# Kernel optimization log

Hardware: AMD Instinct MI355X
Metric: run time of the kernel (lower is better)

## Reference

```python
import jax, jax.numpy as jnp
import numpy as np

B, N, C = 4, 4096, 2048
EPS = 1e-5  # torch.nn.LayerNorm default


def setup_inputs() -> dict:
    key = jax.random.key(0)
    kx, = jax.random.split(key, 1)
    x = jax.random.normal(kx, (B, N, C), dtype=jnp.float32)
    gamma = jnp.ones((C,), dtype=jnp.float32)   # LayerNorm weight
    beta = jnp.zeros((C,), dtype=jnp.float32)   # LayerNorm bias
    return {"x": x, "gamma": gamma, "beta": beta}


def reference(x, gamma, beta):
    # The original repeats x to (B,N,N,C), applies a (no-op on the diagonal)
    # triu mask, FFTs every row over C, and extracts the (n,n) diagonal.
    # The diagonal rows are exactly the unmasked originals, so this equals:
    #   LayerNorm(real(fft(x, axis=-1)))
    y = jnp.fft.fft(x, axis=-1).real  # (B,N,C)
    mu = jnp.mean(y, axis=-1, keepdims=True)
    var = jnp.mean(jnp.square(y - mu), axis=-1, keepdims=True)  # biased, as torch LN
    return (y - mu) * jax.lax.rsqrt(var + EPS) * gamma + beta
```

## Files before the change

kernel.cpp:

```cpp
#include <hip/hip_runtime.h>
#include <math.h>


#define TPB 256
#define CD  2048

__device__ __forceinline__ float2 cadd(float2 a, float2 b){ return make_float2(a.x+b.x, a.y+b.y); }
__device__ __forceinline__ float2 csub(float2 a, float2 b){ return make_float2(a.x-b.x, a.y-b.y); }

__device__ __forceinline__ void dft8(const float2* z, float2* y)
{
    const float C8 = 0.70710678118654752440f;
    float2 a0=cadd(z[0],z[4]), a1=cadd(z[1],z[5]), a2=cadd(z[2],z[6]), a3=cadd(z[3],z[7]);
    float2 b0=csub(z[0],z[4]), b1=csub(z[1],z[5]), b2=csub(z[2],z[6]), b3=csub(z[3],z[7]);
    float2 t1=make_float2(C8*(b1.x+b1.y), C8*(b1.y-b1.x));
    float2 t2=make_float2(b2.y, -b2.x);
    float2 t3=make_float2(C8*(b3.y-b3.x), -C8*(b3.x+b3.y));
    {
        float pr=a0.x+a2.x, pi=a0.y+a2.y, mr=a0.x-a2.x, mi=a0.y-a2.y;
        float qr=a1.x+a3.x, qi=a1.y+a3.y, nr=a1.x-a3.x, ni=a1.y-a3.y;
        y[0]=make_float2(pr+qr,pi+qi); y[2]=make_float2(mr+ni,mi-nr);
        y[4]=make_float2(pr-qr,pi-qi); y[6]=make_float2(mr-ni,mi+nr);
    }
    {
        float pr=b0.x+t2.x, pi=b0.y+t2.y, mr=b0.x-t2.x, mi=b0.y-t2.y;
        float qr=t1.x+t3.x, qi=t1.y+t3.y, nr=t1.x-t3.x, ni=t1.y-t3.y;
        y[1]=make_float2(pr+qr,pi+qi); y[3]=make_float2(mr+ni,mi-nr);
        y[5]=make_float2(pr-qr,pi-qi); y[7]=make_float2(mr-ni,mi+nr);
    }
}

template<int S_, int OFFM>
__device__ __forceinline__ void r8_store(float2* Lw, const float2* y, int p)
{
    Lw[0] = y[0];
    if (S_ == 64 && p == 0) {
#pragma unroll
        for (int r = 1; r < 8; ++r) Lw[OFFM*r] = y[r];
        return;
    }
    const float th = -6.28318530717958647692f * ((float)S_ / 2048.0f);
    float s1, c1;
    __sincosf(th * (float)p, &s1, &c1);
    float cr=c1, sr=s1;
    Lw[OFFM] = make_float2(c1*y[1].x - s1*y[1].y, c1*y[1].y + s1*y[1].x);
#pragma unroll
    for (int r = 2; r < 8; ++r) {
        float cn = cr*c1 - sr*s1, sn = sr*c1 + cr*s1;
        cr=cn; sr=sn;
        Lw[OFFM*r] = make_float2(cr*y[r].x - sr*y[r].y, cr*y[r].y + sr*y[r].x);
    }
}

__global__ __launch_bounds__(TPB, 8) void fourier_ln_kernel(
    const float* __restrict__ x,
    const float* __restrict__ gamma,
    const float* __restrict__ beta,
    float* __restrict__ out)
{
    __shared__ float2 L[2304];
    __shared__ float rmem[20];

    const int t  = threadIdx.x;
    const int t8 = t >> 3;
    const long long row0 = 2LL * (long long)blockIdx.x;
    const float* __restrict__ x0 = x + row0 * CD;
    const float* __restrict__ x1 = x0 + CD;

    float2 z[8], y[8];
#pragma unroll
    for (int r = 0; r < 8; ++r) {
        const int k = t + 256*r;
        z[r] = make_float2(x0[k], x1[k]);
    }

    float2* const Lr = L + (t + t8);

    dft8(z, y);
    r8_store<1, 1>(L + 9*t, y, t);
    __syncthreads();
#pragma unroll
    for (int r = 0; r < 8; ++r) z[r] = Lr[288*r];
    __syncthreads();

    dft8(z, y);
    r8_store<8, 9>(L + ((t & 7) + 72*t8), y, t8);
    __syncthreads();
#pragma unroll
    for (int r = 0; r < 8; ++r) z[r] = Lr[288*r];
    __syncthreads();

    dft8(z, y);
    {
        const int q = t & 63, p = t >> 6;
        r8_store<64, 72>(L + (q + (q >> 3) + 576*p), y, p);
    }
    __syncthreads();
#pragma unroll
    for (int r = 0; r < 8; ++r) z[r] = Lr[288*r];
    __syncthreads();

    float2 Z[8];
    {
        float pr=z[0].x+z[4].x, pi=z[0].y+z[4].y, mr=z[0].x-z[4].x, mi=z[0].y-z[4].y;
        float qr=z[2].x+z[6].x, qi=z[2].y+z[6].y, nr=z[2].x-z[6].x, ni=z[2].y-z[6].y;
        Z[0]=make_float2(pr+qr,pi+qi); Z[2]=make_float2(mr+ni,mi-nr);
        Z[4]=make_float2(pr-qr,pi-qi); Z[6]=make_float2(mr-ni,mi+nr);
    }
    {
        float pr=z[1].x+z[5].x, pi=z[1].y+z[5].y, mr=z[1].x-z[5].x, mi=z[1].y-z[5].y;
        float qr=z[3].x+z[7].x, qi=z[3].y+z[7].y, nr=z[3].x-z[7].x, ni=z[3].y-z[7].y;
        Z[1]=make_float2(pr+qr,pi+qi); Z[3]=make_float2(mr+ni,mi-nr);
        Z[5]=make_float2(pr-qr,pi-qi); Z[7]=make_float2(mr-ni,mi+nr);
    }
#pragma unroll
    for (int j = 0; j < 8; ++j) Lr[288*j] = Z[j];
    __syncthreads();

    float y0v[8], y1v[8];
    float s0=0.f, ss0=0.f, s1=0.f, ss1=0.f;
    const float2* const Ls = L + (4*t + (t >> 1));
#pragma unroll
    for (int h = 0; h < 2; ++h) {
#pragma unroll
        for (int c = 0; c < 4; ++c) {
            const int k  = 4*t + 1024*h + c;
            const int rv = (CD - k) & (CD - 1);
            float2 zk = Ls[c + 1152*h];
            float2 zr = L[rv + (rv >> 3)];
            float a = 0.5f*(zk.x + zr.x);
            float b = 0.5f*(zk.y + zr.y);
            const int i = 4*h + c;
            y0v[i]=a; y1v[i]=b;
            s0+=a; ss0+=a*a; s1+=b; ss1+=b*b;
        }
    }

#pragma unroll
    for (int off = 32; off > 0; off >>= 1) {
        s0  += __shfl_down(s0,  off, 64);
        ss0 += __shfl_down(ss0, off, 64);
        s1  += __shfl_down(s1,  off, 64);
        ss1 += __shfl_down(ss1, off, 64);
    }
    const int wave = t >> 6;
    if ((t & 63) == 0) {
        rmem[4*wave+0]=s0; rmem[4*wave+1]=ss0; rmem[4*wave+2]=s1; rmem[4*wave+3]=ss1;
    }
    __syncthreads();
    if (t == 0) {
        float S0=0.f, SS0=0.f, S1=0.f, SS1=0.f;
#pragma unroll
        for (int w = 0; w < 4; ++w) {
            S0+=rmem[4*w+0]; SS0+=rmem[4*w+1]; S1+=rmem[4*w+2]; SS1+=rmem[4*w+3];
        }
        const float inv = 1.0f/(float)CD;
        float m0=S0*inv, m1=S1*inv;
        rmem[16]=m0; rmem[17]=rsqrtf(SS0*inv - m0*m0 + 1e-5f);
        rmem[18]=m1; rmem[19]=rsqrtf(SS1*inv - m1*m1 + 1e-5f);
    }
    __syncthreads();
    const float mu0=rmem[16], r0=rmem[17], mu1=rmem[18], r1=rmem[19];

    const float4* gv = (const float4*)gamma;
    const float4* bv = (const float4*)beta;
    float4* o0 = (float4*)(out + row0*CD);
    float4* o1 = (float4*)(out + (row0+1)*CD);
#pragma unroll
    for (int h = 0; h < 2; ++h) {
        const int i4 = t + 256*h;
        float4 g  = gv[i4];
        float4 be = bv[i4];
        float4 v0, v1;
        v0.x=(y0v[4*h+0]-mu0)*r0*g.x+be.x; v0.y=(y0v[4*h+1]-mu0)*r0*g.y+be.y;
        v0.z=(y0v[4*h+2]-mu0)*r0*g.z+be.z; v0.w=(y0v[4*h+3]-mu0)*r0*g.w+be.w;
        v1.x=(y1v[4*h+0]-mu1)*r1*g.x+be.x; v1.y=(y1v[4*h+1]-mu1)*r1*g.y+be.y;
        v1.z=(y1v[4*h+2]-mu1)*r1*g.z+be.z; v1.w=(y1v[4*h+3]-mu1)*r1*g.w+be.w;
        o0[i4]=v0; o1[i4]=v1;
    }
}

extern "C" void kernel_launch(void* const* d_in, const int* in_sizes, int n_in,
                              void* d_out, int out_size, void* d_ws, size_t ws_size,
                              hipStream_t stream) {
    (void)in_sizes; (void)n_in; (void)d_ws; (void)ws_size; (void)out_size;
    const float* x     = (const float*)d_in[0];
    const float* gamma = (const float*)d_in[1];
    const float* beta  = (const float*)d_in[2];
    float* out = (float*)d_out;

    const int total_rows = 4 * 4096;
    const int blocks = total_rows / 2;
    fourier_ln_kernel<<<blocks, TPB, 0, stream>>>(x, gamma, beta, out);
}
```

Before: 232.7 us.

## Pair conjugate FFT bins across lanes to drop final LDS round trip and barriers

The last radix-4 stage now reads from a permuted column index so that adjacent lanes hold bins k and N-k. The real-part split uses a lane shuffle instead of writing the spectrum back to LDS and re-reading it, which removes two barriers and an LDS pass. The final statistics are reduced redundantly by every thread, dropping another barrier, and twiddles are computed by squaring instead of a serial recurrence. In exchange, global stores become scalar and strided rather than float4, and gamma/beta are loaded per element.

```diff
diff --git a/kernel.cpp b/kernel.cpp
--- a/kernel.cpp
+++ b/kernel.cpp
@@ -42,14 +42,18 @@
     const float th = -6.28318530717958647692f * ((float)S_ / 2048.0f);
     float s1, c1;
     __sincosf(th * (float)p, &s1, &c1);
-    float cr=c1, sr=s1;
-    Lw[OFFM] = make_float2(c1*y[1].x - s1*y[1].y, c1*y[1].y + s1*y[1].x);
+    const float c2 = c1*c1 - s1*s1, s2 = 2.0f*c1*s1;
+    const float c4 = c2*c2 - s2*s2, s4 = 2.0f*c2*s2;
+    const float c3 = c1*c2 - s1*s2, s3 = s1*c2 + c1*s2;
+    const float c5 = c1*c4 - s1*s4, s5 = s1*c4 + c1*s4;
+    const float c6 = c2*c4 - s2*s4, s6 = s2*c4 + c2*s4;
+    const float c7 = c3*c4 - s3*s4, s7 = s3*c4 + c3*s4;
+    const float cw[8] = {1.f, c1, c2, c3, c4, c5, c6, c7};
+    const float sw[8] = {0.f, s1, s2, s3, s4, s5, s6, s7};
 #pragma unroll
-    for (int r = 2; r < 8; ++r) {
-        float cn = cr*c1 - sr*s1, sn = sr*c1 + cr*s1;
-        cr=cn; sr=sn;
-        Lw[OFFM*r] = make_float2(cr*y[r].x - sr*y[r].y, cr*y[r].y + sr*y[r].x);
-    }
+    for (int r = 1; r < 8; ++r)
+        Lw[OFFM*r] = make_float2(cw[r]*y[r].x - sw[r]*y[r].y,
+                                 cw[r]*y[r].y + sw[r]*y[r].x);
 }
 
 __global__ __launch_bounds__(TPB, 8) void fourier_ln_kernel(
@@ -59,7 +63,7 @@
     float* __restrict__ out)
 {
     __shared__ float2 L[2304];
-    __shared__ float rmem[20];
+    __shared__ float rmem[16];
 
     const int t  = threadIdx.x;
     const int t8 = t >> 3;
@@ -96,9 +100,22 @@
         r8_store<64, 72>(L + (q + (q >> 3) + 576*p), y, p);
     }
     __syncthreads();
+
+    const int u   = t >> 1;
+    const int sig = (t & 1) ? ((u == 0) ? 128 : 256 - u) : u;
+
+    {
+        const float2* Lsig = L + (sig + (sig >> 3));
 #pragma unroll
-    for (int r = 0; r < 8; ++r) z[r] = Lr[288*r];
-    __syncthreads();
+        for (int r = 0; r < 8; ++r) z[r] = Lsig[288*r];
+    }
+
+    float gv[8], bv[8];
+#pragma unroll
+    for (int j = 0; j < 8; ++j) {
+        gv[j] = gamma[sig + 256*j];
+        bv[j] = beta[sig + 256*j];
+    }
 
     float2 Z[8];
     {
@@ -113,27 +130,22 @@
         Z[1]=make_float2(pr+qr,pi+qi); Z[3]=make_float2(mr+ni,mi-nr);
         Z[5]=make_float2(pr-qr,pi-qi); Z[7]=make_float2(mr-ni,mi+nr);
     }
-#pragma unroll
-    for (int j = 0; j < 8; ++j) Lr[288*j] = Z[j];
-    __syncthreads();
 
     float y0v[8], y1v[8];
     float s0=0.f, ss0=0.f, s1=0.f, ss1=0.f;
-    const float2* const Ls = L + (4*t + (t >> 1));
 #pragma unroll
-    for (int h = 0; h < 2; ++h) {
-#pragma unroll
-        for (int c = 0; c < 4; ++c) {
-            const int k  = 4*t + 1024*h + c;
-            const int rv = (CD - k) & (CD - 1);
-            float2 zk = Ls[c + 1152*h];
-            float2 zr = L[rv + (rv >> 3)];
-            float a = 0.5f*(zk.x + zr.x);
-            float b = 0.5f*(zk.y + zr.y);
-            const int i = 4*h + c;
-            y0v[i]=a; y1v[i]=b;
-            s0+=a; ss0+=a*a; s1+=b; ss1+=b*b;
-        }
+    for (int j = 0; j < 8; ++j) {
+        float vx = __shfl_xor(Z[7-j].x, 1, 64);
+        float vy = __shfl_xor(Z[7-j].y, 1, 64);
+        const int ja = (8-j) & 7;
+        float ax = (t == 0) ? Z[ja].x : Z[7-j].x;
+        float ay = (t == 0) ? Z[ja].y : Z[7-j].y;
+        vx = (t < 2) ? ax : vx;
+        vy = (t < 2) ? ay : vy;
+        float a = 0.5f*(Z[j].x + vx);
+        float b = 0.5f*(Z[j].y + vy);
+        y0v[j]=a; y1v[j]=b;
+        s0+=a; ss0+=a*a; s1+=b; ss1+=b*b;
     }
 
 #pragma unroll
@@ -148,35 +160,24 @@
         rmem[4*wave+0]=s0; rmem[4*wave+1]=ss0; rmem[4*wave+2]=s1; rmem[4*wave+3]=ss1;
     }
     __syncthreads();
-    if (t == 0) {
-        float S0=0.f, SS0=0.f, S1=0.f, SS1=0.f;
+    float S0=0.f, SS0=0.f, S1=0.f, SS1=0.f;
 #pragma unroll
-        for (int w = 0; w < 4; ++w) {
-            S0+=rmem[4*w+0]; SS0+=rmem[4*w+1]; S1+=rmem[4*w+2]; SS1+=rmem[4*w+3];
-        }
-        const float inv = 1.0f/(float)CD;
-        float m0=S0*inv, m1=S1*inv;
-        rmem[16]=m0; rmem[17]=rsqrtf(SS0*inv - m0*m0 + 1e-5f);
-        rmem[18]=m1; rmem[19]=rsqrtf(SS1*inv - m1*m1 + 1e-5f);
+    for (int w = 0; w < 4; ++w) {
+        S0+=rmem[4*w+0]; SS0+=rmem[4*w+1]; S1+=rmem[4*w+2]; SS1+=rmem[4*w+3];
     }
-    __syncthreads();
-    const float mu0=rmem[16], r0=rmem[17], mu1=rmem[18], r1=rmem[19];
+    const float inv = 1.0f/(float)CD;
+    const float mu0 = S0*inv, mu1 = S1*inv;
+    const float r0 = rsqrtf(SS0*inv - mu0*mu0 + 1e-5f);
+    const float r1 = rsqrtf(SS1*inv - mu1*mu1 + 1e-5f);
 
-    const float4* gv = (const float4*)gamma;
-    const float4* bv = (const float4*)beta;
-    float4* o0 = (float4*)(out + row0*CD);
-    float4* o1 = (float4*)(out + (row0+1)*CD);
+    float* __restrict__ o0 = out + row0*CD;
+    float* __restrict__ o1 = o0 + CD;
 #pragma unroll
-    for (int h = 0; h < 2; ++h) {
-        const int i4 = t + 256*h;
-        float4 g  = gv[i4];
-        float4 be = bv[i4];
-        float4 v0, v1;
-        v0.x=(y0v[4*h+0]-mu0)*r0*g.x+be.x; v0.y=(y0v[4*h+1]-mu0)*r0*g.y+be.y;
-        v0.z=(y0v[4*h+2]-mu0)*r0*g.z+be.z; v0.w=(y0v[4*h+3]-mu0)*r0*g.w+be.w;
-        v1.x=(y1v[4*h+0]-mu1)*r1*g.x+be.x; v1.y=(y1v[4*h+1]-mu1)*r1*g.y+be.y;
-        v1.z=(y1v[4*h+2]-mu1)*r1*g.z+be.z; v1.w=(y1v[4*h+3]-mu1)*r1*g.w+be.w;
-        o0[i4]=v0; o1[i4]=v1;
+    for (int j = 0; j < 8; ++j) {
+        const int k = sig + 256*j;
+        const float rg0 = r0 * gv[j], rg1 = r1 * gv[j];
+        o0[k] = (y0v[j] - mu0) * rg0 + bv[j];
+        o1[k] = (y1v[j] - mu1) * rg1 + bv[j];
     }
 }
 
```

Measured after the change: 236.9 us. No clear change (+1.8%).
